# Kernel optimization log

Hardware: AMD Instinct MI355X
Metric: run time of the kernel (lower is better)

## Reference

```python
import jax, jax.numpy as jnp
import numpy as np

DIM = 128  # parameter size fixed in __init__


def _rope_rows(x, c):
    """Apply rope_flash to the [c, DIM] matrix formed by repeating x (shape [DIM]) c times.
    axis=0 -> position = arange(c); half_size = DIM // 2."""
    half = DIM // 2
    pos = jnp.arange(c, dtype=jnp.float32)  # [c]
    inv_freq = 10000.0 ** (-(jnp.arange(half, dtype=jnp.float32) / float(half)))  # [half]
    sinusoid = pos[:, None] * inv_freq[None, :]  # [c, half]
    sin = jnp.sin(sinusoid)
    cos = jnp.cos(sinusoid)
    x1 = x[:half]  # [half], constant across rows (row-repeat of the param)
    x2 = x[half:]
    # broadcast [half] against [c, half]
    return jnp.concatenate([x1 * cos - x2 * sin, x2 * cos + x1 * sin], axis=-1)  # [c, DIM]


def setup_inputs() -> dict:
    key = jax.random.key(0)
    ka, kb = jax.random.split(key)
    # truncated_normal_(std=0.02) init approximated with scaled normals (values irrelevant to math)
    a = jax.random.normal(ka, (DIM,), dtype=jnp.float32) * 0.02
    b = jax.random.normal(kb, (DIM,), dtype=jnp.float32) * 0.02
    return {"a": a, "b": b, "c": 8192}


def reference(a, b, c):
    a_rot = _rope_rows(a, c)  # [c, DIM]
    b_rot = _rope_rows(b, c)  # [c, DIM]
    # einsum('mk,nk->mn')
    return jnp.einsum('mk,nk->mn', a_rot, b_rot)  # [c, c]
```

## Files before the change

### kernel.cpp

```cpp
#include <hip/hip_runtime.h>


#define CSEQ 8192
#define HALF 64
#define GOFF (CSEQ - 1)

__global__ __launch_bounds__(256) void compute_g_kernel(
    const float* __restrict__ a, const float* __restrict__ b,
    float* __restrict__ g) {
    const int lane = threadIdx.x & 63;
    const int d    = blockIdx.x * 4 + (threadIdx.x >> 6);
    const int j    = lane;

    float a1 = a[j], a2 = a[j + HALF];
    float b1 = b[j], b2 = b[j + HALF];
    float P = a1 * b1 + a2 * b2;
    float Q = a1 * b2 - a2 * b1;
    float f = exp2f(-0.20762050593046014f * (float)j);
    float s, c;
    sincosf((float)d * f, &s, &c);
    float sP = P * c;
    float sQ = Q * s;

    #pragma unroll
    for (int off = 32; off > 0; off >>= 1) {
        sP += __shfl_down(sP, off, 64);
        sQ += __shfl_down(sQ, off, 64);
    }
    if (lane == 0) {
        g[GOFF + d] = sP + sQ;
        g[GOFF - d] = sP - sQ;
    }
}

__global__ __launch_bounds__(256) void fill_out_kernel(
    const float* __restrict__ g, float* __restrict__ out) {
    __shared__ float lds[1024];
    const unsigned b  = blockIdx.x;
    const unsigned m  = b >> 3;
    const unsigned N0 = (b & 7u) << 10;
    const unsigned t  = threadIdx.x;

    const int lo = (int)(GOFF + m) - (int)N0 - 1023;
    #pragma unroll
    for (int r = 0; r < 4; ++r) {
        int j = r * 256 + (int)t;
        lds[1023 - j] = g[lo + j];
    }
    __syncthreads();

    const unsigned c0 = t << 2;
    float4 v = *reinterpret_cast<const float4*>(&lds[c0]);
    *reinterpret_cast<float4*>(out + (size_t)m * CSEQ + N0 + c0) = v;
}

extern "C" void kernel_launch(void* const* d_in, const int* in_sizes, int n_in,
                              void* d_out, int out_size, void* d_ws, size_t ws_size,
                              hipStream_t stream) {
    const float* a = (const float*)d_in[0];
    const float* b = (const float*)d_in[1];
    float* g   = (float*)d_ws;
    float* out = (float*)d_out;

    compute_g_kernel<<<CSEQ / 4 / 1, 256, 0, stream>>>(a, b, g);

    fill_out_kernel<<<CSEQ * 8, 256, 0, stream>>>(g, out);
}
```

Measured before the change: 254.5 us.

## Replicate shifted Toeplitz vector for aligned float4 copies without LDS

The first kernel now writes four copies of the diagonal vector, each shifted by one element, so every output row's reversed slice starts on a 16-byte boundary. The fill kernel becomes a grid-stride loop of direct float4 global-to-global copies, dropping LDS staging and the barrier. It also launches far fewer blocks. The cost is four times the workspace and extra scattered writes in the small first kernel.

```diff
diff --git a/kernel.cpp b/kernel.cpp
--- a/kernel.cpp
+++ b/kernel.cpp
@@ -3,11 +3,11 @@
 
 #define CSEQ 8192
 #define HALF 64
-#define GOFF (CSEQ - 1)
+#define TSTRIDE 16384
 
 __global__ __launch_bounds__(256) void compute_g_kernel(
     const float* __restrict__ a, const float* __restrict__ b,
-    float* __restrict__ g) {
+    float* __restrict__ T) {
     const int lane = threadIdx.x & 63;
     const int d    = blockIdx.x * 4 + (threadIdx.x >> 6);
     const int j    = lane;
@@ -28,30 +28,33 @@
         sQ += __shfl_down(sQ, off, 64);
     }
     if (lane == 0) {
-        g[GOFF + d] = sP + sQ;
-        g[GOFF - d] = sP - sQ;
+        const float vp = sP + sQ;
+        const float vm = sP - sQ;
+        #pragma unroll
+        for (int sh = 0; sh < 4; ++sh) {
+            const int ip = 8191 - d - sh;
+            if (ip >= 0) T[sh * TSTRIDE + ip] = vp;
+            T[sh * TSTRIDE + (8191 + d - sh)] = vm;
+        }
     }
 }
 
 __global__ __launch_bounds__(256) void fill_out_kernel(
-    const float* __restrict__ g, float* __restrict__ out) {
-    __shared__ float lds[1024];
-    const unsigned b  = blockIdx.x;
-    const unsigned m  = b >> 3;
-    const unsigned N0 = (b & 7u) << 10;
-    const unsigned t  = threadIdx.x;
-
-    const int lo = (int)(GOFF + m) - (int)N0 - 1023;
-    #pragma unroll
-    for (int r = 0; r < 4; ++r) {
-        int j = r * 256 + (int)t;
-        lds[1023 - j] = g[lo + j];
+    const float* __restrict__ T, float* __restrict__ out) {
+    const unsigned tid = blockIdx.x * 256u + threadIdx.x;
+    float4* __restrict__ out4 = reinterpret_cast<float4*>(out);
+    #pragma unroll 8
+    for (int it = 0; it < 32; ++it) {
+        const unsigned q    = tid + (unsigned)it * 524288u;
+        const unsigned m    = q >> 11;
+        const unsigned colq = q & 2047u;
+        const unsigned r    = 8191u - m;
+        const unsigned sh   = r & 3u;
+        const unsigned b4   = r >> 2;
+        const float4* Tp = reinterpret_cast<const float4*>(T + sh * TSTRIDE);
+        const float4 v = Tp[b4 + colq];
+        out4[q] = v;
     }
-    __syncthreads();
-
-    const unsigned c0 = t << 2;
-    float4 v = *reinterpret_cast<const float4*>(&lds[c0]);
-    *reinterpret_cast<float4*>(out + (size_t)m * CSEQ + N0 + c0) = v;
 }
 
 extern "C" void kernel_launch(void* const* d_in, const int* in_sizes, int n_in,
@@ -59,10 +62,10 @@
                               hipStream_t stream) {
     const float* a = (const float*)d_in[0];
     const float* b = (const float*)d_in[1];
-    float* g   = (float*)d_ws;
+    float* T   = (float*)d_ws;
     float* out = (float*)d_out;
 
-    compute_g_kernel<<<CSEQ / 4 / 1, 256, 0, stream>>>(a, b, g);
+    compute_g_kernel<<<CSEQ / 4, 256, 0, stream>>>(a, b, T);
 
-    fill_out_kernel<<<CSEQ * 8, 256, 0, stream>>>(g, out);
+    fill_out_kernel<<<2048, 256, 0, stream>>>(T, out);
 }
```

Measured after the change: 268.5 us. 5.5% more time.
